# Optimization experiments

Measured on AMD Instinct MI355X. Metric: run time of the kernel, lower is better.

Reference implementation:

```python
import jax, jax.numpy as jnp
import numpy as np

IN_F = 4096
OUT_F = 4096

def setup_inputs() -> dict:
    key = jax.random.key(0)
    k1, k2 = jax.random.split(key)
    x = jax.random.normal(k1, (8, 2048, IN_F), dtype=jnp.float32)
    weight = jax.random.normal(k2, (OUT_F, IN_F), dtype=jnp.float32) * 0.1
    bias = jnp.zeros((OUT_F,), dtype=jnp.float32)
    return {"x": x, "weight": weight, "bias": bias}

def reference(x, weight, bias):
    # binarize weights to +-1 with per-row abs-mean scale
    binary_w = jnp.sign(weight)
    scale = jnp.mean(jnp.abs(weight), axis=1, keepdims=True)  # [OUT_F, 1]
    w = scale * binary_w
    # F.linear: x @ w.T + bias
    return jnp.einsum('bsi,oi->bso', x, w) + bias
```

## Files before the change

kernel.cpp:

```cpp
#include <hip/hip_runtime.h>
#include <hip/hip_bf16.h>

#define M_TOT 16384
#define N_TOT 4096
#define K_TOT 4096

typedef __attribute__((ext_vector_type(8))) short bf16x8;
typedef __attribute__((ext_vector_type(4))) float f32x4;

typedef const __attribute__((address_space(1))) void* gptr_t;
typedef __attribute__((address_space(3))) void* lptr_t;

__device__ inline unsigned short f2bf(float f) {
    union { float f; unsigned u; } v; v.f = f;
    unsigned u = v.u;
    u += 0x7FFFu + ((u >> 16) & 1u);
    return (unsigned short)(u >> 16);
}

__device__ inline unsigned short sgn_bf(float f) {
    union { float f; unsigned u; } v; v.f = f;
    return (unsigned short)(((v.u >> 16) & 0x8000u) | 0x3F80u);
}

__global__ void prep_weight(const float* __restrict__ w,
                            unsigned short* __restrict__ bw,
                            float* __restrict__ scale) {
    const int row = blockIdx.x;
    const int tid = threadIdx.x;
    const float4* wr = (const float4*)(w + (size_t)row * K_TOT);
    float s = 0.f;
#pragma unroll
    for (int i = 0; i < 4; ++i) {
        int idx = tid + i * 256;
        float4 v = wr[idx];
        s += fabsf(v.x) + fabsf(v.y) + fabsf(v.z) + fabsf(v.w);
        if (bw) {
            ushort4 b;
            b.x = sgn_bf(v.x); b.y = sgn_bf(v.y);
            b.z = sgn_bf(v.z); b.w = sgn_bf(v.w);
            *(ushort4*)(bw + (size_t)row * K_TOT + idx * 4) = b;
        }
    }
#pragma unroll
    for (int off = 32; off > 0; off >>= 1) s += __shfl_down(s, off, 64);
    __shared__ float red[4];
    if ((tid & 63) == 0) red[tid >> 6] = s;
    __syncthreads();
    if (tid == 0) scale[row] = (red[0] + red[1] + red[2] + red[3]) * (1.f / (float)K_TOT);
}

__global__ void conv_x(const float* __restrict__ x, unsigned short* __restrict__ xb) {
    const long n4 = (long)M_TOT * K_TOT / 4;
    long i = (long)blockIdx.x * blockDim.x + threadIdx.x;
    const long stride = (long)gridDim.x * blockDim.x;
    for (; i < n4; i += stride) {
        float4 v = ((const float4*)x)[i];
        ushort4 b;
        b.x = f2bf(v.x); b.y = f2bf(v.y); b.z = f2bf(v.z); b.w = f2bf(v.w);
        ((ushort4*)xb)[i] = b;
    }
}

#define AS0 0
#define BS0 16384
#define AS1 32768
#define BS1 49152

#define STAGE(Mat, row0, ldsbase, h, ktv)                                         \
  {                                                                               \
    _Pragma("unroll")                                                             \
    for (int c_ = 0; c_ < 2; ++c_) {                                              \
      const unsigned short* g_ = (Mat) +                                          \
          (size_t)((row0) + (h)*128 + c_*64 + wv*8 + srow) * K_TOT + (ktv) + scol;\
      __builtin_amdgcn_global_load_lds((gptr_t)g_,                                \
          (lptr_t)(lds + (ldsbase) + ((h)*128 + c_*64 + wv*8) * 64), 16, 0, 0);   \
    }                                                                             \
  }

#define DS_A(h, base)                                                             \
  {                                                                               \
    _Pragma("unroll")                                                             \
    for (int i_ = 0; i_ < 4; ++i_) {                                              \
      _Pragma("unroll")                                                           \
      for (int k_ = 0; k_ < 2; ++k_) {                                            \
        int off_ = (wr*128 + (h)*64 + i_*16 + l16)*128 + k_*64 + quad*16;         \
        off_ ^= ((off_ >> 7) & 7) << 4;                                           \
        af[i_][k_] = *(const bf16x8*)((const char*)(lds + (base)) + off_);        \
      }                                                                           \
    }                                                                             \
  }

#define DS_B(dst, g, base)                                                        \
  {                                                                               \
    _Pragma("unroll")                                                             \
    for (int j_ = 0; j_ < 2; ++j_) {                                              \
      _Pragma("unroll")                                                           \
      for (int k_ = 0; k_ < 2; ++k_) {                                            \
        int ob_ = (wc*64 + (g)*32 + j_*16 + l16)*128 + k_*64 + quad*16;           \
        ob_ ^= ((ob_ >> 7) & 7) << 4;                                             \
        dst[j_][k_] = *(const bf16x8*)((const char*)(lds + (base)) + ob_);        \
      }                                                                           \
    }                                                                             \
  }

#define MMA(h, g, bset)                                                           \
  {                                                                               \
    __builtin_amdgcn_s_setprio(1);                                                \
    _Pragma("unroll")                                                             \
    for (int i_ = 0; i_ < 4; ++i_) {                                              \
      _Pragma("unroll")                                                           \
      for (int j_ = 0; j_ < 2; ++j_) {                                            \
        acc[(h)*4+i_][(g)*2+j_] = __builtin_amdgcn_mfma_f32_16x16x32_bf16(        \
            af[i_][0], bset[j_][0], acc[(h)*4+i_][(g)*2+j_], 0, 0, 0);            \
        acc[(h)*4+i_][(g)*2+j_] = __builtin_amdgcn_mfma_f32_16x16x32_bf16(        \
            af[i_][1], bset[j_][1], acc[(h)*4+i_][(g)*2+j_], 0, 0, 0);            \
      }                                                                           \
    }                                                                             \
    __builtin_amdgcn_s_setprio(0);                                                \
  }

#define BAR1  { __builtin_amdgcn_s_barrier(); asm volatile("s_waitcnt lgkmcnt(0)"); }
#define BAR2  { __builtin_amdgcn_s_barrier(); }
#define VM4   { asm volatile("s_waitcnt vmcnt(4)" ::: "memory"); }
#define VM0   { asm volatile("s_waitcnt vmcnt(0)" ::: "memory"); }

__global__ __launch_bounds__(512, 2) void gemm_bin_8ph(
    const unsigned short* __restrict__ A,
    const unsigned short* __restrict__ B,
    const float* __restrict__ scale,
    const float* __restrict__ bias,
    float* __restrict__ out) {
    __shared__ unsigned short lds[4 * 16384];

    const int tid  = threadIdx.x;
    const int wv   = tid >> 6;
    const int lane = tid & 63;
    const int quad = lane >> 4;
    const int l16  = lane & 15;
    const int wr   = wv >> 2;
    const int wc   = wv & 3;

    int bid = blockIdx.x;
    bid = (bid & 7) * 128 + (bid >> 3);
    const int bn = (bid & 15) * 256;
    const int bm = (bid >> 4) * 256;

    const int srow = lane >> 3;
    const int scol = (((lane & 7) ^ ((lane >> 3) & 7)) * 8);

    f32x4 acc[8][4] = {};
    bf16x8 af[4][2], bl[2][2], bh[2][2];

    STAGE(A, bm, AS0, 0, 0)
    STAGE(A, bm, AS0, 1, 0)
    STAGE(B, bn, BS0, 0, 0)
    STAGE(B, bn, BS0, 1, 0)
    STAGE(B, bn, BS1, 0, 64)
    STAGE(B, bn, BS1, 1, 64)
    asm volatile("s_waitcnt vmcnt(4)" ::: "memory");
    __builtin_amdgcn_s_barrier();

    int kt = 0;
#pragma unroll 1
    for (int t = 0; t < (K_TOT / 128) - 1; ++t, kt += 128) {
        DS_A(0, AS0) DS_B(bl, 0, BS0)
        STAGE(A, bm, AS1, 0, kt + 64)
        BAR1 MMA(0, 0, bl) BAR2
        DS_B(bh, 1, BS0)
        STAGE(A, bm, AS1, 1, kt + 64)
        BAR1 MMA(0, 1, bh) BAR2
        DS_A(1, AS0)
        STAGE(B, bn, BS0, 0, kt + 128)
        BAR1 MMA(1, 1, bh) BAR2
        STAGE(B, bn, BS0, 1, kt + 128)
        BAR1 MMA(1, 0, bl) VM4 BAR2
        DS_A(0, AS1) DS_B(bl, 0, BS1)
        STAGE(A, bm, AS0, 0, kt + 128)
        BAR1 MMA(0, 0, bl) BAR2
        DS_B(bh, 1, BS1)
        STAGE(A, bm, AS0, 1, kt + 128)
        BAR1 MMA(0, 1, bh) BAR2
        DS_A(1, AS1)
        STAGE(B, bn, BS1, 0, kt + 192)
        BAR1 MMA(1, 1, bh) BAR2
        STAGE(B, bn, BS1, 1, kt + 192)
        BAR1 MMA(1, 0, bl) VM4 BAR2
    }

    DS_A(0, AS0) DS_B(bl, 0, BS0)
    STAGE(A, bm, AS1, 0, kt + 64)
    BAR1 MMA(0, 0, bl) BAR2
    DS_B(bh, 1, BS0)
    STAGE(A, bm, AS1, 1, kt + 64)
    BAR1 MMA(0, 1, bh) BAR2
    DS_A(1, AS0)
    BAR1 MMA(1, 1, bh) BAR2
    BAR1 MMA(1, 0, bl) VM0 BAR2
    DS_A(0, AS1) DS_B(bl, 0, BS1)
    BAR1 MMA(0, 0, bl) BAR2
    DS_B(bh, 1, BS1)
    BAR1 MMA(0, 1, bh) BAR2
    DS_A(1, AS1)
    BAR1 MMA(1, 1, bh) BAR2
    BAR1 MMA(1, 0, bl)

#pragma unroll
    for (int j4 = 0; j4 < 4; ++j4) {
        const int gn = bn + wc * 64 + j4 * 16 + l16;
        const float sc = scale[gn];
        const float bi = bias[gn];
#pragma unroll
        for (int i8 = 0; i8 < 8; ++i8) {
            const int gm0 = bm + wr * 128 + i8 * 16 + quad * 4;
#pragma unroll
            for (int r = 0; r < 4; ++r)
                out[(size_t)(gm0 + r) * N_TOT + gn] = acc[i8][j4][r] * sc + bi;
        }
    }
}

__global__ __launch_bounds__(256) void gemm_bin_fb(const float* __restrict__ A,
                                                   const float* __restrict__ Bf,
                                                   const float* __restrict__ scale,
                                                   const float* __restrict__ bias,
                                                   float* __restrict__ out) {
    __shared__ unsigned short As[128][40];
    __shared__ unsigned short Bs[128][40];

    const int tid  = threadIdx.x;
    const int wave = tid >> 6;
    const int lane = tid & 63;
    const int quad = lane >> 4;
    const int l16  = lane & 15;
    const int wr   = wave >> 1;
    const int wc   = wave & 1;
    const int bn   = blockIdx.x * 128;
    const int bm   = blockIdx.y * 128;

    f32x4 acc[4][4] = {};

    for (int kt = 0; kt < K_TOT; kt += 32) {
        const int row0 = tid >> 3;
        const int c4   = (tid & 7) * 4;
#pragma unroll
        for (int p = 0; p < 4; ++p) {
            int row = row0 + p * 32;
            float4 v = *(const float4*)(A + (size_t)(bm + row) * K_TOT + kt + c4);
            ushort4 b;
            b.x = f2bf(v.x); b.y = f2bf(v.y); b.z = f2bf(v.z); b.w = f2bf(v.w);
            *(ushort4*)&As[row][c4] = b;
        }
#pragma unroll
        for (int p = 0; p < 4; ++p) {
            int row = row0 + p * 32;
            float4 v = *(const float4*)(Bf + (size_t)(bn + row) * K_TOT + kt + c4);
            ushort4 b;
            b.x = sgn_bf(v.x); b.y = sgn_bf(v.y);
            b.z = sgn_bf(v.z); b.w = sgn_bf(v.w);
            *(ushort4*)&Bs[row][c4] = b;
        }
        __syncthreads();

        bf16x8 af2[4], bfr[4];
#pragma unroll
        for (int i = 0; i < 4; ++i)
            af2[i] = *(const bf16x8*)&As[wr * 64 + i * 16 + l16][quad * 8];
#pragma unroll
        for (int j = 0; j < 4; ++j)
            bfr[j] = *(const bf16x8*)&Bs[wc * 64 + j * 16 + l16][quad * 8];
#pragma unroll
        for (int i = 0; i < 4; ++i)
#pragma unroll
            for (int j = 0; j < 4; ++j)
                acc[i][j] = __builtin_amdgcn_mfma_f32_16x16x32_bf16(af2[i], bfr[j], acc[i][j], 0, 0, 0);
        __syncthreads();
    }

#pragma unroll
    for (int j = 0; j < 4; ++j) {
        const int gn = bn + wc * 64 + j * 16 + l16;
        const float sc = scale[gn];
        const float bi = bias[gn];
#pragma unroll
        for (int i = 0; i < 4; ++i) {
            const int gm0 = bm + wr * 64 + i * 16 + quad * 4;
#pragma unroll
            for (int r = 0; r < 4; ++r)
                out[(size_t)(gm0 + r) * N_TOT + gn] = acc[i][j][r] * sc + bi;
        }
    }
}

extern "C" void kernel_launch(void* const* d_in, const int* in_sizes, int n_in,
                              void* d_out, int out_size, void* d_ws, size_t ws_size,
                              hipStream_t stream) {
    const float* x    = (const float*)d_in[0];
    const float* w    = (const float*)d_in[1];
    const float* bias = (const float*)d_in[2];
    float* out        = (float*)d_out;

    const size_t off_scale = 0;
    const size_t off_bw    = 16384;
    const size_t off_xb    = off_bw + (size_t)N_TOT * K_TOT * 2;
    const size_t need_full = off_xb + (size_t)M_TOT * K_TOT * 2;

    float* scale = (float*)((char*)d_ws + off_scale);
    const bool full = ws_size >= need_full;

    if (full) {
        unsigned short* bw = (unsigned short*)((char*)d_ws + off_bw);
        unsigned short* xb = (unsigned short*)((char*)d_ws + off_xb);
        prep_weight<<<N_TOT, 256, 0, stream>>>(w, bw, scale);
        conv_x<<<8192, 256, 0, stream>>>(x, xb);
        const int nwg = (M_TOT / 256) * (N_TOT / 256);
        gemm_bin_8ph<<<nwg, 512, 0, stream>>>(xb, bw, scale, bias, out);
    } else {
        prep_weight<<<N_TOT, 256, 0, stream>>>(w, nullptr, scale);
        dim3 grid(N_TOT / 128, M_TOT / 128);
        gemm_bin_fb<<<grid, 256, 0, stream>>>(x, w, scale, bias, out);
    }
}
```

Baseline: 894.8 us.

## Issue A-tile loads one phase earlier and widen x conversion stores

The GEMM main loop now issues the A-half loads for the next buffer one phase earlier, including an extra A stage in the prologue. The vmcnt wait rises from 4 to 6 outstanding loads so more global-to-LDS traffic stays in flight across barriers. Separately, the fp32-to-bf16 conversion kernel now processes 8 elements per thread with 16-byte stores and half as many blocks. The deeper prefetch must still respect the LDS buffer reuse order; a mistake there would give wrong results or stalls.

```diff
diff --git a/kernel.cpp b/kernel.cpp
--- a/kernel.cpp
+++ b/kernel.cpp
@@ -50,15 +50,20 @@
     if (tid == 0) scale[row] = (red[0] + red[1] + red[2] + red[3]) * (1.f / (float)K_TOT);
 }
 
-__global__ void conv_x(const float* __restrict__ x, unsigned short* __restrict__ xb) {
-    const long n4 = (long)M_TOT * K_TOT / 4;
+__global__ void conv_x(const float* __restrict__ x, unsigned int* __restrict__ xb) {
+    const long n = (long)M_TOT * K_TOT / 8;
     long i = (long)blockIdx.x * blockDim.x + threadIdx.x;
     const long stride = (long)gridDim.x * blockDim.x;
-    for (; i < n4; i += stride) {
-        float4 v = ((const float4*)x)[i];
-        ushort4 b;
-        b.x = f2bf(v.x); b.y = f2bf(v.y); b.z = f2bf(v.z); b.w = f2bf(v.w);
-        ((ushort4*)xb)[i] = b;
+    const float4* x4 = (const float4*)x;
+    for (; i < n; i += stride) {
+        float4 a = x4[2 * i];
+        float4 b = x4[2 * i + 1];
+        uint4 o;
+        o.x = ((unsigned)f2bf(a.y) << 16) | f2bf(a.x);
+        o.y = ((unsigned)f2bf(a.w) << 16) | f2bf(a.z);
+        o.z = ((unsigned)f2bf(b.y) << 16) | f2bf(b.x);
+        o.w = ((unsigned)f2bf(b.w) << 16) | f2bf(b.z);
+        ((uint4*)xb)[i] = o;
     }
 }
 
@@ -122,7 +127,7 @@
 
 #define BAR1  { __builtin_amdgcn_s_barrier(); asm volatile("s_waitcnt lgkmcnt(0)"); }
 #define BAR2  { __builtin_amdgcn_s_barrier(); }
-#define VM4   { asm volatile("s_waitcnt vmcnt(4)" ::: "memory"); }
+#define VM6   { asm volatile("s_waitcnt vmcnt(6)" ::: "memory"); }
 #define VM0   { asm volatile("s_waitcnt vmcnt(0)" ::: "memory"); }
 
 __global__ __launch_bounds__(512, 2) void gemm_bin_8ph(
@@ -157,42 +162,42 @@
     STAGE(B, bn, BS0, 0, 0)
     STAGE(B, bn, BS0, 1, 0)
     STAGE(B, bn, BS1, 0, 64)
+    STAGE(A, bm, AS1, 0, 64)
     STAGE(B, bn, BS1, 1, 64)
-    asm volatile("s_waitcnt vmcnt(4)" ::: "memory");
+    VM6
     __builtin_amdgcn_s_barrier();
 
     int kt = 0;
 #pragma unroll 1
     for (int t = 0; t < (K_TOT / 128) - 1; ++t, kt += 128) {
         DS_A(0, AS0) DS_B(bl, 0, BS0)
-        STAGE(A, bm, AS1, 0, kt + 64)
+        STAGE(A, bm, AS1, 1, kt + 64)
         BAR1 MMA(0, 0, bl) BAR2
         DS_B(bh, 1, BS0)
-        STAGE(A, bm, AS1, 1, kt + 64)
         BAR1 MMA(0, 1, bh) BAR2
         DS_A(1, AS0)
         STAGE(B, bn, BS0, 0, kt + 128)
         BAR1 MMA(1, 1, bh) BAR2
+        STAGE(A, bm, AS0, 0, kt + 128)
         STAGE(B, bn, BS0, 1, kt + 128)
-        BAR1 MMA(1, 0, bl) VM4 BAR2
+        BAR1 MMA(1, 0, bl) VM6 BAR2
         DS_A(0, AS1) DS_B(bl, 0, BS1)
-        STAGE(A, bm, AS0, 0, kt + 128)
+        STAGE(A, bm, AS0, 1, kt + 128)
         BAR1 MMA(0, 0, bl) BAR2
         DS_B(bh, 1, BS1)
-        STAGE(A, bm, AS0, 1, kt + 128)
         BAR1 MMA(0, 1, bh) BAR2
         DS_A(1, AS1)
         STAGE(B, bn, BS1, 0, kt + 192)
         BAR1 MMA(1, 1, bh) BAR2
+        STAGE(A, bm, AS1, 0, kt + 192)
         STAGE(B, bn, BS1, 1, kt + 192)
-        BAR1 MMA(1, 0, bl) VM4 BAR2
+        BAR1 MMA(1, 0, bl) VM6 BAR2
     }
 
     DS_A(0, AS0) DS_B(bl, 0, BS0)
-    STAGE(A, bm, AS1, 0, kt + 64)
+    STAGE(A, bm, AS1, 1, kt + 64)
     BAR1 MMA(0, 0, bl) BAR2
     DS_B(bh, 1, BS0)
-    STAGE(A, bm, AS1, 1, kt + 64)
     BAR1 MMA(0, 1, bh) BAR2
     DS_A(1, AS0)
     BAR1 MMA(1, 1, bh) BAR2
@@ -312,7 +317,7 @@
         unsigned short* bw = (unsigned short*)((char*)d_ws + off_bw);
         unsigned short* xb = (unsigned short*)((char*)d_ws + off_xb);
         prep_weight<<<N_TOT, 256, 0, stream>>>(w, bw, scale);
-        conv_x<<<8192, 256, 0, stream>>>(x, xb);
+        conv_x<<<4096, 256, 0, stream>>>(x, (unsigned int*)xb);
         const int nwg = (M_TOT / 256) * (N_TOT / 256);
         gemm_bin_8ph<<<nwg, 512, 0, stream>>>(xb, bw, scale, bias, out);
     } else {
```

Measured after the change: 914.7 us. 2.2% more time.
